# Kernel tuning notes

Hardware: AMD Instinct MI355X
Metric: run time of the kernel (lower is better)

The kernel has to match this reference:

```python
import jax, jax.numpy as jnp
import numpy as np

B, S, C = 1, 2048, 2048
H, D = 16, 128
FF = 8192
EPS = 1e-6


def _rms(x, w):
    return x * jax.lax.rsqrt(jnp.mean(x * x, axis=-1, keepdims=True) + EPS) * w


def _rope(x, cos, sin):
    # x: [B,S,H,D]; cos/sin: [S,D]
    x1, x2 = jnp.split(x, 2, axis=-1)
    rot = jnp.concatenate([-x2, x1], axis=-1)
    return x * cos[None, :, None, :] + rot * sin[None, :, None, :]


def setup_inputs() -> dict:
    key = jax.random.key(0)
    ks = jax.random.split(key, 12)
    # RoPE tables
    inv_freq = 1.0 / (10000.0 ** (jnp.arange(0, D, 2, dtype=jnp.float32) / D))
    freqs = jnp.arange(S, dtype=jnp.float32)[:, None] * inv_freq[None, :]
    emb = jnp.concatenate([freqs, freqs], axis=-1)  # [S,D]
    # causal additive mask
    causal = jnp.tril(jnp.ones((S, S), dtype=bool))
    mask = jnp.where(causal, 0.0, -1e9).astype(jnp.float32)[None, None]
    w = lambda k, shp: (jax.random.normal(k, shp, dtype=jnp.float32) * 0.02)
    return {
        "hidden_states": jax.random.normal(ks[0], (B, S, C), dtype=jnp.float32),
        "cos": jnp.cos(emb),
        "sin": jnp.sin(emb),
        "attention_mask": mask,
        "ln1_w": jnp.ones((C,), dtype=jnp.float32),
        "wq": w(ks[1], (C, C)),
        "wk": w(ks[2], (C, C)),
        "wv": w(ks[3], (C, C)),
        "wo": w(ks[4], (C, C)),
        "ln2_w": jnp.ones((C,), dtype=jnp.float32),
        "w_gate": w(ks[5], (FF, C)),
        "w_up": w(ks[6], (FF, C)),
        "w_down": w(ks[7], (C, FF)),
    }


def reference(hidden_states, cos, sin, attention_mask, ln1_w, wq, wk, wv, wo,
              ln2_w, w_gate, w_up, w_down):
    # --- input RMSNorm ---
    x = _rms(hidden_states, ln1_w)
    # --- W2 (Gaussian-kernel) attention ---
    q = (x @ wq.T).reshape(B, S, H, D)
    k = (x @ wk.T).reshape(B, S, H, D)
    v = (x @ wv.T).reshape(B, S, H, D)
    q = _rope(q, cos, sin).transpose(0, 2, 1, 3)  # [B,H,S,D]
    k = _rope(k, cos, sin).transpose(0, 2, 1, 3)
    v = v.transpose(0, 2, 1, 3)
    qk = jnp.einsum('bhid,bhjd->bhij', q, k)
    q2 = jnp.sum(q * q, axis=-1)  # [B,H,S]
    k2 = jnp.sum(k * k, axis=-1)
    dist2 = q2[..., :, None] - 2.0 * qk + k2[..., None, :]  # ||q-k||^2
    scores = -dist2 / (2.0 * np.sqrt(D).astype(np.float32)) + attention_mask
    attn = jax.nn.softmax(scores, axis=-1)
    ctx = jnp.einsum('bhij,bhjd->bhid', attn, v)
    attn_out = ctx.transpose(0, 2, 1, 3).reshape(B, S, C) @ wo.T
    h = hidden_states + attn_out
    # --- post-attn RMSNorm + SwiGLU FFN ---
    y = _rms(h, ln2_w)
    ffn = (jax.nn.silu(y @ w_gate.T) * (y @ w_up.T)) @ w_down.T
    return h + ffn
```

## Files before the change

kernel.cpp:

```cpp
#include <hip/hip_runtime.h>
#include <cstdint>
#include <cstddef>

typedef __bf16 bf16x8 __attribute__((ext_vector_type(8)));
typedef float f32x4 __attribute__((ext_vector_type(4)));

union V16 { uint4 u; bf16x8 b; unsigned short s[8]; };

__device__ __forceinline__ float b2f(unsigned short u) {
  unsigned int x = ((unsigned int)u) << 16;
  float f;
  __builtin_memcpy(&f, &x, 4);
  return f;
}
__device__ __forceinline__ unsigned short f2b(float f) {
  unsigned int u;
  __builtin_memcpy(&u, &f, 4);
  u = u + 0x7FFFu + ((u >> 16) & 1u);
  return (unsigned short)(u >> 16);
}

__device__ __forceinline__ f32x4 mfma16(bf16x8 a, bf16x8 b, f32x4 c) {
  return __builtin_amdgcn_mfma_f32_16x16x32_bf16(a, b, c, 0, 0, 0);
}

__device__ __forceinline__ void gld_lds16(const unsigned short* g, unsigned short* l) {
  __builtin_amdgcn_global_load_lds((__attribute__((address_space(1))) void*)g,
                                   (__attribute__((address_space(3))) void*)l,
                                   16, 0, 0);
}

__global__ __launch_bounds__(256) void cvt_k(const float* __restrict__ in,
                                             unsigned short* __restrict__ out, int n) {
  const int i = (blockIdx.x * 256 + threadIdx.x) * 4;
  if (i + 3 < n) {
    const float4 v = *(const float4*)(in + i);
    ushort4 o;
    o.x = f2b(v.x); o.y = f2b(v.y); o.z = f2b(v.z); o.w = f2b(v.w);
    *(ushort4*)(out + i) = o;
  }
}

__global__ __launch_bounds__(256) void rms_k(const float* __restrict__ xin,
                                             const float* __restrict__ wgt,
                                             unsigned short* __restrict__ out) {
  const int s = blockIdx.x;
  const int t = threadIdx.x;
  float vals[8];
  float ss = 0.f;
#pragma unroll
  for (int i = 0; i < 8; ++i) {
    const int c = t + i * 256;
    const float f = xin[(size_t)s * 2048 + c];
    vals[i] = f;
    ss += f * f;
  }
#pragma unroll
  for (int off = 32; off > 0; off >>= 1) ss += __shfl_xor(ss, off);
  __shared__ float red[4];
  if ((t & 63) == 0) red[t >> 6] = ss;
  __syncthreads();
  ss = red[0] + red[1] + red[2] + red[3];
  const float sc = rsqrtf(ss * (1.f / 2048.f) + 1e-6f);
#pragma unroll
  for (int i = 0; i < 8; ++i) {
    const int c = t + i * 256;
    out[(size_t)s * 2048 + c] = f2b(vals[i] * sc * wgt[c]);
  }
}

__global__ __launch_bounds__(256) void rope_qk(unsigned short* qb, unsigned short* kb,
                                               const float* __restrict__ cosb,
                                               const float* __restrict__ sinb,
                                               float* __restrict__ k2c) {
  const int idx = blockIdx.x * 256 + threadIdx.x;
  const int d = idx & 63;
  const int h = (idx >> 6) & 15;
  const int s = idx >> 10;
  const size_t base = (size_t)s * 2048 + h * 128;
  const int cb = s * 128;
  const float c1 = cosb[cb + d],      s1 = sinb[cb + d];
  const float c2 = cosb[cb + d + 64], s2 = sinb[cb + d + 64];
  {
    const float x1 = b2f(qb[base + d]), x2 = b2f(qb[base + d + 64]);
    qb[base + d]      = f2b(x1 * c1 - x2 * s1);
    qb[base + d + 64] = f2b(x2 * c2 + x1 * s2);
  }
  {
    const float x1 = b2f(kb[base + d]), x2 = b2f(kb[base + d + 64]);
    const float k1 = x1 * c1 - x2 * s1;
    const float k2 = x2 * c2 + x1 * s2;
    kb[base + d]      = f2b(k1);
    kb[base + d + 64] = f2b(k2);
    float ss = k1 * k1 + k2 * k2;
#pragma unroll
    for (int off = 32; off > 0; off >>= 1) ss += __shfl_xor(ss, off);
    if (d == 0) k2c[h * 2048 + s] = ss * 0.04419417382415922f;
  }
}

template <int EPI, int RT>
__global__ __launch_bounds__(256, 2) void gemm_nt(
    const unsigned short* __restrict__ A,
    const unsigned short* __restrict__ B0,
    const unsigned short* __restrict__ B1,
    const unsigned short* __restrict__ B2,
    unsigned short* C0, unsigned short* C1, unsigned short* C2,
    const unsigned short* auxb, const float* auxf, float* Cf,
    int N, int K) {
  constexpr int TM = RT * 32;
  constexpr int APASS = TM / 64;
  const unsigned short* B = (blockIdx.z == 0) ? B0 : (blockIdx.z == 1 ? B1 : B2);
  unsigned short* C = (blockIdx.z == 0) ? C0 : (blockIdx.z == 1 ? C1 : C2);

  const int m0 = blockIdx.y * TM;
  const int n0 = blockIdx.x * 128;
  const int t = threadIdx.x;
  const int lane = t & 63;
  const int w = t >> 6;
  const int quad = lane >> 4;
  const int l15 = lane & 15;
  const int wr = w >> 1;
  const int wc = w & 1;

  __shared__ __align__(16) unsigned short As[TM * 32];
  __shared__ __align__(16) unsigned short Bs[128 * 32];

  const f32x4 vzero = {0.f, 0.f, 0.f, 0.f};
  f32x4 acc[RT][4];
#pragma unroll
  for (int i = 0; i < RT; ++i)
#pragma unroll
    for (int j = 0; j < 4; ++j) acc[i][j] = vzero;

  const int srow = w * 16 + (lane >> 2);
  const int scol = (lane & 3) * 8;
  const unsigned short* Ag = A + (size_t)(m0 + srow) * K + scol;
  const unsigned short* Bg = B + (size_t)(n0 + srow) * K + scol;

  for (int k0 = 0; k0 < K; k0 += 32) {
#pragma unroll
    for (int p = 0; p < APASS; ++p)
      gld_lds16(Ag + (size_t)p * 64 * K + k0, As + p * 2048 + w * 512);
#pragma unroll
    for (int p = 0; p < 2; ++p)
      gld_lds16(Bg + (size_t)p * 64 * K + k0, Bs + p * 2048 + w * 512);
    __syncthreads();

    bf16x8 af[RT], bfr[4];
#pragma unroll
    for (int rt = 0; rt < RT; ++rt)
      af[rt] = *(const bf16x8*)&As[(wr * (RT * 16) + rt * 16 + l15) * 32 + quad * 8];
#pragma unroll
    for (int ct = 0; ct < 4; ++ct)
      bfr[ct] = *(const bf16x8*)&Bs[(wc * 64 + ct * 16 + l15) * 32 + quad * 8];
#pragma unroll
    for (int rt = 0; rt < RT; ++rt)
#pragma unroll
      for (int ct = 0; ct < 4; ++ct)
        acc[rt][ct] = mfma16(af[rt], bfr[ct], acc[rt][ct]);
    __syncthreads();
  }

#pragma unroll
  for (int rt = 0; rt < RT; ++rt) {
#pragma unroll
    for (int ct = 0; ct < 4; ++ct) {
#pragma unroll
      for (int r = 0; r < 4; ++r) {
        const int m = m0 + wr * (RT * 16) + rt * 16 + quad * 4 + r;
        const int n = n0 + wc * 64 + ct * 16 + l15;
        const size_t idx = (size_t)m * N + n;
        const float a = acc[rt][ct][r];
        if constexpr (EPI == 0) {
          C[idx] = f2b(a);
        } else if constexpr (EPI == 1) {
          Cf[idx] = auxf[idx] + a;
        } else {
          const float g = b2f(auxb[idx]);
          const float sg = g / (1.f + __expf(-g));
          C[idx] = f2b(sg * a);
        }
      }
    }
  }
}

__global__ __launch_bounds__(256, 3) void flash_w2(
    const unsigned short* __restrict__ q,
    const unsigned short* __restrict__ kk,
    const unsigned short* __restrict__ v,
    const float* __restrict__ k2c,
    unsigned short* __restrict__ ctx) {
  constexpr int Cw = 2048;
  constexpr float TWOC = 0.08838834764831843f;
  const int h = blockIdx.y;
  const int i = (h >= 8) ? (31 - blockIdx.x) : blockIdx.x;
  const int i0 = i * 64;
  const int t = threadIdx.x;
  const int lane = t & 63;
  const int w = t >> 6;
  const int quad = lane >> 4;
  const int l15 = lane & 15;

  __shared__ __align__(16) unsigned short Ks[64 * 136];
  __shared__ __align__(16) unsigned short VTs[128 * 72];
  __shared__ __align__(16) unsigned short Ps[4][16 * 72];

  bf16x8 aq[4];
  {
    const unsigned short* qp = q + (size_t)(i0 + w * 16 + l15) * Cw + h * 128;
#pragma unroll
    for (int kt = 0; kt < 4; ++kt) {
      V16 u;
      u.u = *(const uint4*)(qp + kt * 32 + quad * 8);
      aq[kt] = u.b;
    }
  }

  const f32x4 vzero = {0.f, 0.f, 0.f, 0.f};
  f32x4 o[8];
#pragma unroll
  for (int nt = 0; nt < 8; ++nt) o[nt] = vzero;
  float mrow[4] = {-1e30f, -1e30f, -1e30f, -1e30f};
  float lrow[4] = {0.f, 0.f, 0.f, 0.f};

  const int njt = i + 1;
  const int jr = t >> 2;
  const int c0 = (t & 3) * 32;
  const int jlo = jr & 7;
  const int jhi = jr >> 3;
  for (int jt = 0; jt < njt; ++jt) {
    const int j0 = jt * 64;
    __syncthreads();
    {
      const unsigned short* kp = kk + (size_t)(j0 + jr) * Cw + h * 128 + c0;
      const unsigned short* vp = v + (size_t)(j0 + jr) * Cw + h * 128 + c0;
#pragma unroll
      for (int ii = 0; ii < 4; ++ii) {
        *(uint4*)&Ks[jr * 136 + c0 + ii * 8] = *(const uint4*)(kp + ii * 8);
        V16 vu;
        vu.u = *(const uint4*)(vp + ii * 8);
#pragma unroll
        for (int e = 0; e < 8; ++e) {
          const int dd = c0 + ii * 8 + e;
          const int gs = (jhi ^ (dd >> 4)) & 7;
          VTs[dd * 72 + (jlo | (gs << 3))] = vu.s[e];
        }
      }
    }
    __syncthreads();

    float k2v[4];
#pragma unroll
    for (int ct = 0; ct < 4; ++ct) k2v[ct] = k2c[h * 2048 + j0 + ct * 16 + l15];

    f32x4 sc[4];
#pragma unroll
    for (int ct = 0; ct < 4; ++ct) {
      f32x4 a = vzero;
#pragma unroll
      for (int kt = 0; kt < 4; ++kt) {
        V16 u;
        u.u = *(const uint4*)&Ks[(ct * 16 + l15) * 136 + kt * 32 + quad * 8];
        a = mfma16(aq[kt], u.b, a);
      }
      sc[ct] = a;
    }

    const bool diag = (jt == njt - 1);
#pragma unroll
    for (int ct = 0; ct < 4; ++ct) {
#pragma unroll
      for (int r = 0; r < 4; ++r) {
        float s = fmaf(TWOC, sc[ct][r], -k2v[ct]);
        if (diag) {
          const int gi = w * 16 + quad * 4 + r;
          const int gj = ct * 16 + l15;
          s = (gj <= gi) ? s : -1e30f;
        }
        sc[ct][r] = s;
      }
    }

    float al[4];
#pragma unroll
    for (int r = 0; r < 4; ++r) {
      float rm = fmaxf(fmaxf(sc[0][r], sc[1][r]), fmaxf(sc[2][r], sc[3][r]));
      rm = fmaxf(rm, __shfl_xor(rm, 1));
      rm = fmaxf(rm, __shfl_xor(rm, 2));
      rm = fmaxf(rm, __shfl_xor(rm, 4));
      rm = fmaxf(rm, __shfl_xor(rm, 8));
      const float mn = fmaxf(mrow[r], rm);
      al[r] = __expf(mrow[r] - mn);
      mrow[r] = mn;
      float ps = 0.f;
#pragma unroll
      for (int ct = 0; ct < 4; ++ct) {
        const float p = __expf(sc[ct][r] - mn);
        sc[ct][r] = p;
        ps += p;
      }
      ps += __shfl_xor(ps, 1);
      ps += __shfl_xor(ps, 2);
      ps += __shfl_xor(ps, 4);
      ps += __shfl_xor(ps, 8);
      lrow[r] = lrow[r] * al[r] + ps;
    }
#pragma unroll
    for (int nt = 0; nt < 8; ++nt)
#pragma unroll
      for (int r = 0; r < 4; ++r) o[nt][r] *= al[r];

#pragma unroll
    for (int ct = 0; ct < 4; ++ct)
#pragma unroll
      for (int r = 0; r < 4; ++r)
        Ps[w][(quad * 4 + r) * 72 + ct * 16 + l15] = f2b(sc[ct][r]);

#pragma unroll
    for (int kt2 = 0; kt2 < 2; ++kt2) {
      V16 pa;
      pa.u = *(const uint4*)&Ps[w][l15 * 72 + kt2 * 32 + quad * 8];
#pragma unroll
      for (int nt = 0; nt < 8; ++nt) {
        V16 vb;
        const int dd = nt * 16 + l15;
        const int gs = (kt2 * 4 + quad) ^ nt;
        vb.u = *(const uint4*)&VTs[dd * 72 + gs * 8];
        o[nt] = mfma16(pa.b, vb.b, o[nt]);
      }
    }
  }

  float invl[4];
#pragma unroll
  for (int r = 0; r < 4; ++r) invl[r] = 1.f / lrow[r];
#pragma unroll
  for (int nt = 0; nt < 8; ++nt) {
#pragma unroll
    for (int r = 0; r < 4; ++r) {
      const int gi = i0 + w * 16 + quad * 4 + r;
      ctx[(size_t)gi * Cw + h * 128 + nt * 16 + l15] = f2b(o[nt][r] * invl[r]);
    }
  }
}

extern "C" void kernel_launch(void* const* d_in, const int* in_sizes, int n_in,
                              void* d_out, int out_size, void* d_ws, size_t ws_size,
                              hipStream_t stream) {
  (void)in_sizes; (void)n_in; (void)out_size; (void)ws_size;
  const float* hid  = (const float*)d_in[0];
  const float* cosb = (const float*)d_in[1];
  const float* sinb = (const float*)d_in[2];
  const float* ln1w = (const float*)d_in[4];
  const float* wq   = (const float*)d_in[5];
  const float* wk   = (const float*)d_in[6];
  const float* wv   = (const float*)d_in[7];
  const float* wo   = (const float*)d_in[8];
  const float* ln2w = (const float*)d_in[9];
  const float* wg   = (const float*)d_in[10];
  const float* wu   = (const float*)d_in[11];
  const float* wd   = (const float*)d_in[12];
  float* outp = (float*)d_out;

  const size_t SC = (size_t)2048 * 2048;
  const size_t FC = (size_t)8192 * 2048;
  unsigned short* p = (unsigned short*)d_ws;
  unsigned short* wqb = p;  p += SC;
  unsigned short* wkb = p;  p += SC;
  unsigned short* wvb = p;  p += SC;
  unsigned short* wob = p;  p += SC;
  unsigned short* wgb = p;  p += FC;
  unsigned short* wub = p;  p += FC;
  unsigned short* wdb = p;  p += FC;
  unsigned short* xn  = p;  p += SC;
  unsigned short* qb  = p;  p += SC;
  unsigned short* kb  = p;  p += SC;
  unsigned short* vb  = p;  p += SC;
  unsigned short* ctxb = p; p += SC;
  float* hf = (float*)p;   p += 2 * SC;
  float* k2cb = (float*)p;
  unsigned short* yn = xn;
  unsigned short* gb = qb;

  cvt_k<<<(int)(SC / 1024), 256, 0, stream>>>(wq, wqb, (int)SC);
  cvt_k<<<(int)(SC / 1024), 256, 0, stream>>>(wk, wkb, (int)SC);
  cvt_k<<<(int)(SC / 1024), 256, 0, stream>>>(wv, wvb, (int)SC);
  cvt_k<<<(int)(SC / 1024), 256, 0, stream>>>(wo, wob, (int)SC);
  cvt_k<<<(int)(FC / 1024), 256, 0, stream>>>(wg, wgb, (int)FC);
  cvt_k<<<(int)(FC / 1024), 256, 0, stream>>>(wu, wub, (int)FC);
  cvt_k<<<(int)(FC / 1024), 256, 0, stream>>>(wd, wdb, (int)FC);

  rms_k<<<2048, 256, 0, stream>>>(hid, ln1w, xn);
  gemm_nt<0, 4><<<dim3(16, 16, 3), 256, 0, stream>>>(xn, wqb, wkb, wvb, qb, kb, vb,
                                                     nullptr, nullptr, nullptr, 2048, 2048);
  rope_qk<<<8192, 256, 0, stream>>>(qb, kb, cosb, sinb, k2cb);
  flash_w2<<<dim3(32, 16), 256, 0, stream>>>(qb, kb, vb, k2cb, ctxb);
  gemm_nt<1, 2><<<dim3(16, 32, 1), 256, 0, stream>>>(ctxb, wob, wob, wob,
                                                     nullptr, nullptr, nullptr,
                                                     nullptr, hid, hf, 2048, 2048);
  rms_k<<<2048, 256, 0, stream>>>(hf, ln2w, yn);
  gemm_nt<0, 4><<<dim3(64, 16, 1), 256, 0, stream>>>(yn, wgb, wgb, wgb, gb, gb, gb,
                                                     nullptr, nullptr, nullptr, 8192, 2048);
  gemm_nt<2, 4><<<dim3(64, 16, 1), 256, 0, stream>>>(yn, wub, wub, wub, gb, gb, gb,
                                                     gb, nullptr, nullptr, 8192, 2048);
  gemm_nt<1, 2><<<dim3(16, 32, 1), 256, 0, stream>>>(gb, wdb, wdb, wdb,
                                                     nullptr, nullptr, nullptr,
                                                     nullptr, hf, outp, 2048, 8192);
}
```

Before: 844.5 us.

## Fuse gate/up GEMMs, split-K down projection, merge weight conversion launches

```diff
diff --git a/kernel.cpp b/kernel.cpp
--- a/kernel.cpp
+++ b/kernel.cpp
@@ -30,15 +30,31 @@
                                    16, 0, 0);
 }
 
-__global__ __launch_bounds__(256) void cvt_k(const float* __restrict__ in,
-                                             unsigned short* __restrict__ out, int n) {
-  const int i = (blockIdx.x * 256 + threadIdx.x) * 4;
-  if (i + 3 < n) {
-    const float4 v = *(const float4*)(in + i);
-    ushort4 o;
-    o.x = f2b(v.x); o.y = f2b(v.y); o.z = f2b(v.z); o.w = f2b(v.w);
-    *(ushort4*)(out + i) = o;
-  }
+__global__ __launch_bounds__(256) void cvt_all(const float* __restrict__ wq,
+                                               const float* __restrict__ wk,
+                                               const float* __restrict__ wv,
+                                               const float* __restrict__ wo,
+                                               const float* __restrict__ wg,
+                                               const float* __restrict__ wu,
+                                               const float* __restrict__ wd,
+                                               unsigned short* __restrict__ dst) {
+  const int b = blockIdx.x;
+  const float* src;
+  if (b < 16384) {
+    const int w = b >> 12;
+    src = (w == 0 ? wq : w == 1 ? wk : w == 2 ? wv : wo) + (size_t)(b & 4095) * 1024;
+  } else if (b < 32768) {
+    src = wg + (size_t)(b - 16384) * 1024;
+  } else if (b < 49152) {
+    src = wu + (size_t)(b - 32768) * 1024;
+  } else {
+    src = wd + (size_t)(b - 49152) * 1024;
+  }
+  const int o = threadIdx.x * 4;
+  const float4 v = *(const float4*)(src + o);
+  ushort4 r;
+  r.x = f2b(v.x); r.y = f2b(v.y); r.z = f2b(v.z); r.w = f2b(v.w);
+  *(ushort4*)(dst + (size_t)b * 1024 + o) = r;
 }
 
 __global__ __launch_bounds__(256) void rms_k(const float* __restrict__ xin,
@@ -106,12 +122,21 @@
     const unsigned short* __restrict__ B1,
     const unsigned short* __restrict__ B2,
     unsigned short* C0, unsigned short* C1, unsigned short* C2,
-    const unsigned short* auxb, const float* auxf, float* Cf,
-    int N, int K) {
+    const float* auxf, float* Cf,
+    int N, int K, int kstride) {
   constexpr int TM = RT * 32;
   constexpr int APASS = TM / 64;
-  const unsigned short* B = (blockIdx.z == 0) ? B0 : (blockIdx.z == 1 ? B1 : B2);
-  unsigned short* C = (blockIdx.z == 0) ? C0 : (blockIdx.z == 1 ? C1 : C2);
+  const unsigned short* B;
+  unsigned short* C;
+  size_t koff = 0;
+  if constexpr (EPI == 0) {
+    B = (blockIdx.z == 0) ? B0 : (blockIdx.z == 1 ? B1 : B2);
+    C = (blockIdx.z == 0) ? C0 : (blockIdx.z == 1 ? C1 : C2);
+  } else {
+    B = B0;
+    C = C0;
+    if constexpr (EPI == 3) koff = (size_t)blockIdx.z * K;
+  }
 
   const int m0 = blockIdx.y * TM;
   const int n0 = blockIdx.x * 128;
@@ -135,16 +160,16 @@
 
   const int srow = w * 16 + (lane >> 2);
   const int scol = (lane & 3) * 8;
-  const unsigned short* Ag = A + (size_t)(m0 + srow) * K + scol;
-  const unsigned short* Bg = B + (size_t)(n0 + srow) * K + scol;
+  const unsigned short* Ag = A + (size_t)(m0 + srow) * kstride + scol + koff;
+  const unsigned short* Bg = B + (size_t)(n0 + srow) * kstride + scol + koff;
 
   for (int k0 = 0; k0 < K; k0 += 32) {
 #pragma unroll
     for (int p = 0; p < APASS; ++p)
-      gld_lds16(Ag + (size_t)p * 64 * K + k0, As + p * 2048 + w * 512);
+      gld_lds16(Ag + (size_t)p * 64 * kstride + k0, As + p * 2048 + w * 512);
 #pragma unroll
     for (int p = 0; p < 2; ++p)
-      gld_lds16(Bg + (size_t)p * 64 * K + k0, Bs + p * 2048 + w * 512);
+      gld_lds16(Bg + (size_t)p * 64 * kstride + k0, Bs + p * 2048 + w * 512);
     __syncthreads();
 
     bf16x8 af[RT], bfr[4];
@@ -161,6 +186,10 @@
         acc[rt][ct] = mfma16(af[rt], bfr[ct], acc[rt][ct]);
     __syncthreads();
   }
+
+  float* Cfz = Cf;
+  if constexpr (EPI == 3)
+    Cfz = Cf + (size_t)blockIdx.z * (size_t)gridDim.y * TM * N;
 
 #pragma unroll
   for (int rt = 0; rt < RT; ++rt) {
@@ -177,13 +206,103 @@
         } else if constexpr (EPI == 1) {
           Cf[idx] = auxf[idx] + a;
         } else {
-          const float g = b2f(auxb[idx]);
-          const float sg = g / (1.f + __expf(-g));
-          C[idx] = f2b(sg * a);
+          Cfz[idx] = a;
         }
       }
     }
   }
+}
+
+__global__ __launch_bounds__(256, 2) void gemm_nt2(
+    const unsigned short* __restrict__ A,
+    const unsigned short* __restrict__ B0,
+    const unsigned short* __restrict__ B1,
+    unsigned short* __restrict__ C,
+    int N, int K) {
+  const int m0 = blockIdx.y * 128;
+  const int n0 = blockIdx.x * 128;
+  const int t = threadIdx.x;
+  const int lane = t & 63;
+  const int w = t >> 6;
+  const int quad = lane >> 4;
+  const int l15 = lane & 15;
+  const int wr = w >> 1;
+  const int wc = w & 1;
+
+  __shared__ __align__(16) unsigned short As[128 * 32];
+  __shared__ __align__(16) unsigned short B0s[128 * 32];
+  __shared__ __align__(16) unsigned short B1s[128 * 32];
+
+  const f32x4 vzero = {0.f, 0.f, 0.f, 0.f};
+  f32x4 acc0[4][4], acc1[4][4];
+#pragma unroll
+  for (int i = 0; i < 4; ++i)
+#pragma unroll
+    for (int j = 0; j < 4; ++j) { acc0[i][j] = vzero; acc1[i][j] = vzero; }
+
+  const int srow = w * 16 + (lane >> 2);
+  const int scol = (lane & 3) * 8;
+  const unsigned short* Ag  = A  + (size_t)(m0 + srow) * K + scol;
+  const unsigned short* B0g = B0 + (size_t)(n0 + srow) * K + scol;
+  const unsigned short* B1g = B1 + (size_t)(n0 + srow) * K + scol;
+
+  for (int k0 = 0; k0 < K; k0 += 32) {
+#pragma unroll
+    for (int p = 0; p < 2; ++p) {
+      gld_lds16(Ag  + (size_t)p * 64 * K + k0, As  + p * 2048 + w * 512);
+      gld_lds16(B0g + (size_t)p * 64 * K + k0, B0s + p * 2048 + w * 512);
+      gld_lds16(B1g + (size_t)p * 64 * K + k0, B1s + p * 2048 + w * 512);
+    }
+    __syncthreads();
+
+    bf16x8 af[4], b0f[4], b1f[4];
+#pragma unroll
+    for (int rt = 0; rt < 4; ++rt)
+      af[rt] = *(const bf16x8*)&As[(wr * 64 + rt * 16 + l15) * 32 + quad * 8];
+#pragma unroll
+    for (int ct = 0; ct < 4; ++ct) {
+      b0f[ct] = *(const bf16x8*)&B0s[(wc * 64 + ct * 16 + l15) * 32 + quad * 8];
+      b1f[ct] = *(const bf16x8*)&B1s[(wc * 64 + ct * 16 + l15) * 32 + quad * 8];
+    }
+#pragma unroll
+    for (int rt = 0; rt < 4; ++rt)
+#pragma unroll
+      for (int ct = 0; ct < 4; ++ct) {
+        acc0[rt][ct] = mfma16(af[rt], b0f[ct], acc0[rt][ct]);
+        acc1[rt][ct] = mfma16(af[rt], b1f[ct], acc1[rt][ct]);
+      }
+    __syncthreads();
+  }
+
+#pragma unroll
+  for (int rt = 0; rt < 4; ++rt) {
+#pragma unroll
+    for (int ct = 0; ct < 4; ++ct) {
+#pragma unroll
+      for (int r = 0; r < 4; ++r) {
+        const int m = m0 + wr * 64 + rt * 16 + quad * 4 + r;
+        const int n = n0 + wc * 64 + ct * 16 + l15;
+        const float g = acc0[rt][ct][r];
+        const float u = acc1[rt][ct][r];
+        const float sg = g / (1.f + __expf(-g));
+        C[(size_t)m * N + n] = f2b(sg * u);
+      }
+    }
+  }
+}
+
+__global__ __launch_bounds__(256) void comb_k(const float* __restrict__ q0,
+                                              const float* __restrict__ q1,
+                                              const float* __restrict__ hf,
+                                              float* __restrict__ out) {
+  const int i = (blockIdx.x * 256 + threadIdx.x) * 4;
+  const float4 a = *(const float4*)(q0 + i);
+  const float4 b = *(const float4*)(q1 + i);
+  const float4 c = *(const float4*)(hf + i);
+  float4 r;
+  r.x = a.x + b.x + c.x; r.y = a.y + b.y + c.y;
+  r.z = a.z + b.z + c.z; r.w = a.w + b.w + c.w;
+  *(float4*)(out + i) = r;
 }
 
 __global__ __launch_bounds__(256, 3) void flash_w2(
@@ -383,29 +502,22 @@
   float* k2cb = (float*)p;
   unsigned short* yn = xn;
   unsigned short* gb = qb;
-
-  cvt_k<<<(int)(SC / 1024), 256, 0, stream>>>(wq, wqb, (int)SC);
-  cvt_k<<<(int)(SC / 1024), 256, 0, stream>>>(wk, wkb, (int)SC);
-  cvt_k<<<(int)(SC / 1024), 256, 0, stream>>>(wv, wvb, (int)SC);
-  cvt_k<<<(int)(SC / 1024), 256, 0, stream>>>(wo, wob, (int)SC);
-  cvt_k<<<(int)(FC / 1024), 256, 0, stream>>>(wg, wgb, (int)FC);
-  cvt_k<<<(int)(FC / 1024), 256, 0, stream>>>(wu, wub, (int)FC);
-  cvt_k<<<(int)(FC / 1024), 256, 0, stream>>>(wd, wdb, (int)FC);
+  float* qpart = (float*)wqb;
+
+  cvt_all<<<65536, 256, 0, stream>>>(wq, wk, wv, wo, wg, wu, wd, wqb);
 
   rms_k<<<2048, 256, 0, stream>>>(hid, ln1w, xn);
   gemm_nt<0, 4><<<dim3(16, 16, 3), 256, 0, stream>>>(xn, wqb, wkb, wvb, qb, kb, vb,
-                                                     nullptr, nullptr, nullptr, 2048, 2048);
+                                                     nullptr, nullptr, 2048, 2048, 2048);
   rope_qk<<<8192, 256, 0, stream>>>(qb, kb, cosb, sinb, k2cb);
   flash_w2<<<dim3(32, 16), 256, 0, stream>>>(qb, kb, vb, k2cb, ctxb);
   gemm_nt<1, 2><<<dim3(16, 32, 1), 256, 0, stream>>>(ctxb, wob, wob, wob,
                                                      nullptr, nullptr, nullptr,
-                                                     nullptr, hid, hf, 2048, 2048);
+                                                     hid, hf, 2048, 2048, 2048);
   rms_k<<<2048, 256, 0, stream>>>(hf, ln2w, yn);
-  gemm_nt<0, 4><<<dim3(64, 16, 1), 256, 0, stream>>>(yn, wgb, wgb, wgb, gb, gb, gb,
-                                                     nullptr, nullptr, nullptr, 8192, 2048);
-  gemm_nt<2, 4><<<dim3(64, 16, 1), 256, 0, stream>>>(yn, wub, wub, wub, gb, gb, gb,
-                                                     gb, nullptr, nullptr, 8192, 2048);
-  gemm_nt<1, 2><<<dim3(16, 32, 1), 256, 0, stream>>>(gb, wdb, wdb, wdb,
+  gemm_nt2<<<dim3(64, 16), 256, 0, stream>>>(yn, wgb, wub, gb, 8192, 2048);
+  gemm_nt<3, 4><<<dim3(16, 16, 2), 256, 0, stream>>>(gb, wdb, wdb, wdb,
                                                      nullptr, nullptr, nullptr,
-                                                     nullptr, hf, outp, 2048, 8192);
-}
+                                                     nullptr, qpart, 2048, 4096, 8192);
+  comb_k<<<4096, 256, 0, stream>>>(qpart, qpart + SC, hf, outp);
+}
```

Result: faster. 809.5 us (-4.1%).
